# Kernel tuning notes

Hardware: AMD Instinct MI355X
Metric: run time of the kernel (lower is better)

Reference implementation:

```python
import jax, jax.numpy as jnp
import numpy as np

NUM_HEADS = 16
TOP_K = 32
NEG_INF = -1e9
EPS = 1e-8


def setup_inputs() -> dict:
    key = jax.random.key(0)
    ks = jax.random.split(key, 12)
    B, S, D = 2, 1024, 1024
    M, dk = 8192, D // NUM_HEADS
    w = lambda k: jax.random.normal(k, (D, D), jnp.float32) * 0.02
    return {
        "x": jax.random.normal(ks[0], (B, S, D), jnp.float32),
        "Wq": w(ks[1]), "bq": jnp.zeros((D,), jnp.float32),
        "Wk": w(ks[2]), "bk": jnp.zeros((D,), jnp.float32),
        "Wv": w(ks[3]), "bv": jnp.zeros((D,), jnp.float32),
        "Wo": w(ks[4]), "bo": jnp.zeros((D,), jnp.float32),
        "mem_keys": jax.random.normal(ks[5], (M, dk), jnp.float32),
        "mem_vals": jax.random.normal(ks[6], (M, dk), jnp.float32),
        "gate": jnp.zeros((1,), jnp.float32),
    }


def _normalize(v):
    return v / (jnp.linalg.norm(v, axis=-1, keepdims=True) + EPS)


def reference(x, Wq, bq, Wk, bk, Wv, bv, Wo, bo, mem_keys, mem_vals, gate):
    B, S, D = x.shape
    H = NUM_HEADS
    dk = D // H
    # projections (torch Linear: x @ W.T + b), split heads -> [B,H,S,dk]
    split = lambda t: t.reshape(B, S, H, dk).transpose(0, 2, 1, 3)
    q = split(x @ Wq.T + bq)
    k = split(x @ Wk.T + bk)
    v = split(x @ Wv.T + bv)
    # causal attention
    scores = jnp.einsum("bhqd,bhkd->bhqk", q, k) / jnp.sqrt(jnp.float32(dk))
    causal = jnp.triu(jnp.ones((S, S), bool), k=1)  # True above diagonal
    scores = jnp.where(causal, NEG_INF, scores)
    attn = jax.nn.softmax(scores, axis=-1)
    attn_out = jnp.einsum("bhqk,bhkd->bhqd", attn, v)
    attn_out = attn_out.transpose(0, 2, 1, 3).reshape(B, S, D)
    attn_out = attn_out @ Wo.T + bo
    # KNN memory retrieval on flattened per-head queries [B*H*S, dk]
    flat_q = q.reshape(-1, dk)
    sims = _normalize(flat_q) @ _normalize(mem_keys).T  # [Q, M]
    top_scores, idx = jax.lax.top_k(sims, TOP_K)        # [Q, K]
    gathered = mem_vals[idx]                            # [Q, K, dk]
    memory_out = jnp.sum(gathered * top_scores[..., None], axis=-2)  # [Q, dk]
    memory_out = memory_out.reshape(B, H, S, dk).transpose(0, 2, 1, 3).reshape(B, S, D)
    memory_out = memory_out @ Wo.T + bo
    g = jax.nn.sigmoid(gate)
    return g * memory_out + (1.0 - g) * attn_out
```

## Files before the change

kernel.cpp:

```cpp
#include <hip/hip_runtime.h>
#include <stdint.h>
#include <math.h>

#define BATCH   2
#define SEQ     1024
#define DMODEL  1024
#define NHEADS  16
#define DK      64
#define MKEYS   8192
#define NQ      (BATCH*NHEADS*SEQ)
#define THRC    2.25f
#define KPART   4
#define PKEYS2  (MKEYS/KPART)
#define PCAP    64
#define QCAP2   (KPART*PCAP)

typedef __attribute__((ext_vector_type(8))) short short8;
typedef __attribute__((ext_vector_type(4))) float f32x4;
typedef __attribute__((ext_vector_type(2))) double f64x2;
typedef __attribute__((ext_vector_type(4))) double f64x4;

__device__ __forceinline__ short f2bf(float f) {
  uint32_t u = __builtin_bit_cast(uint32_t, f);
  u = (u + 0x7fffu + ((u >> 16) & 1u)) >> 16;
  return (short)u;
}
__device__ __forceinline__ short8 ld_bf8_f32(const float* p) {
  float4 a = *(const float4*)p; float4 b = *(const float4*)(p + 4);
  short8 r;
  r[0]=f2bf(a.x); r[1]=f2bf(a.y); r[2]=f2bf(a.z); r[3]=f2bf(a.w);
  r[4]=f2bf(b.x); r[5]=f2bf(b.y); r[6]=f2bf(b.z); r[7]=f2bf(b.w);
  return r;
}

__device__ __forceinline__ unsigned long long packP(double v, int id) {
  unsigned long long b = __builtin_bit_cast(unsigned long long, v);
  b = (b & 0x8000000000000000ull) ? ~b : (b | 0x8000000000000000ull);
  return (b & ~0x1FFFull) | (unsigned long long)(8191 - id);
}
__device__ __forceinline__ double unpackV(unsigned long long P) {
  unsigned long long K = P & ~0x1FFFull;
  unsigned long long bits = (K & 0x8000000000000000ull) ? (K ^ 0x8000000000000000ull) : ~K;
  return __builtin_bit_cast(double, bits);
}

__global__ __launch_bounds__(256) void norm_keys(const float* __restrict__ mk,
                                                 double* __restrict__ knorm64,
                                                 uint16_t* __restrict__ knbf) {
  int wave = threadIdx.x >> 6, lane = threadIdx.x & 63;
  int m = blockIdx.x * 4 + wave;
  double v = (double)mk[(size_t)m * DK + lane];
  double ss = v * v;
  #pragma unroll
  for (int off = 1; off < 64; off <<= 1) ss += __shfl_xor(ss, off);
  double nv = v / (sqrt(ss) + 1e-8);
  knorm64[(size_t)m * DK + lane] = nv;
  knbf[(size_t)m * DK + lane] = (uint16_t)f2bf((float)nv);
}

__device__ __forceinline__ bool probe_decode(const f64x4 d, int base, int mul,
                                             int out[4]) {
  bool ok = true;
  #pragma unroll
  for (int r = 0; r < 4; r++) {
    int v = (int)d[r];
    int t = v - base;
    bool o = ((double)v == d[r]) && (t >= 0) && (t % mul == 0) && ((t / mul) < 16);
    out[r] = t / mul;
    ok = ok && o;
  }
  return ok;
}

__global__ __launch_bounds__(256, 4) void q64_gemm(const float* __restrict__ x,
                                                   const float* __restrict__ Wq,
                                                   const float* __restrict__ bq,
                                                   double* __restrict__ q64q,
                                                   float* __restrict__ qf32,
                                                   uint16_t* __restrict__ qb) {
  __shared__ __align__(16) float Xs[64 * 68];
  __shared__ __align__(16) float Ws[64 * 68];
  int tid = threadIdx.x, lane = tid & 63, w = tid >> 6;
  int bm = blockIdx.y * 64;
  int h = blockIdx.x;

  f64x4 z = {0.0, 0.0, 0.0, 0.0};
  f64x4 d1 = __builtin_amdgcn_mfma_f64_16x16x4f64((double)lane, 1.0, z, 0, 0, 0);
  f64x4 d2 = __builtin_amdgcn_mfma_f64_16x16x4f64(1.0, (double)lane, z, 0, 0, 0);
  int rdec[4], cdec[4];
  bool ok = probe_decode(d1, 96, 4, rdec);
  bool h1A = (bool)__all(ok ? 1 : 0);
  if (!h1A) ok = probe_decode(d1, 6, 16, rdec);
  bool aOK = h1A || (bool)__all(ok ? 1 : 0);
  ok = probe_decode(d2, 96, 4, cdec);
  bool h1B = (bool)__all(ok ? 1 : 0);
  if (!h1B) ok = probe_decode(d2, 6, 16, cdec);
  bool bOK = h1B || (bool)__all(ok ? 1 : 0);
  int iA = h1A ? (lane & 15) : (lane >> 2);
  int kA = h1A ? (lane >> 4) : (lane & 3);
  int jB = h1B ? (lane & 15) : (lane >> 2);
  int kB = h1B ? (lane >> 4) : (lane & 3);
  bool mfma_ok = aOK && bOK;
  if (mfma_ok) {
    f64x4 d3 = __builtin_amdgcn_mfma_f64_16x16x4f64(
        (double)(4 * iA + kA), (double)(jB + 16 * kB), z, 0, 0, 0);
    bool ok3 = true;
    #pragma unroll
    for (int r = 0; r < 4; r++)
      ok3 = ok3 && (d3[r] == (double)(16 * rdec[r] * cdec[r] + 384 * rdec[r] +
                                      6 * cdec[r] + 224));
    mfma_ok = (bool)__all(ok3 ? 1 : 0);
  }

  if (mfma_ok) {
    int wm = (w >> 1) * 32, wn = (w & 1) * 32;
    f64x4 acc[2][2] = {};
    for (int kt = 0; kt < 16; kt++) {
      __syncthreads();
      #pragma unroll
      for (int i = 0; i < 4; i++) {
        int c4 = tid + 256 * i;
        int r = c4 >> 4, q4 = c4 & 15;
        *(float4*)(Xs + r * 68 + q4 * 4) =
            *(const float4*)(x + (size_t)(bm + r) * DMODEL + kt * 64 + q4 * 4);
        *(float4*)(Ws + r * 68 + q4 * 4) =
            *(const float4*)(Wq + (size_t)(h * 64 + r) * DMODEL + kt * 64 + q4 * 4);
      }
      __syncthreads();
      #pragma unroll
      for (int k = 0; k < 64; k += 4) {
        double a0 = (double)Xs[(wm + iA) * 68 + k + kA];
        double a1 = (double)Xs[(wm + 16 + iA) * 68 + k + kA];
        double b0 = (double)Ws[(wn + jB) * 68 + k + kB];
        double b1 = (double)Ws[(wn + 16 + jB) * 68 + k + kB];
        acc[0][0] = __builtin_amdgcn_mfma_f64_16x16x4f64(a0, b0, acc[0][0], 0, 0, 0);
        acc[0][1] = __builtin_amdgcn_mfma_f64_16x16x4f64(a0, b1, acc[0][1], 0, 0, 0);
        acc[1][0] = __builtin_amdgcn_mfma_f64_16x16x4f64(a1, b0, acc[1][0], 0, 0, 0);
        acc[1][1] = __builtin_amdgcn_mfma_f64_16x16x4f64(a1, b1, acc[1][1], 0, 0, 0);
      }
    }
    #pragma unroll
    for (int mi = 0; mi < 2; mi++)
      #pragma unroll
      for (int ni = 0; ni < 2; ni++)
        #pragma unroll
        for (int rg = 0; rg < 4; rg++) {
          int m = bm + wm + mi * 16 + rdec[rg];
          int d = wn + ni * 16 + cdec[rg];
          int b = m >> 10, s = m & 1023;
          size_t qidx = (((size_t)(b * NHEADS + h) * SEQ) + s) * DK + d;
          double val = acc[mi][ni][rg] + (double)bq[h * DK + d];
          q64q[qidx] = val;
          float fv = (float)val;
          qf32[qidx] = fv;
          qb[qidx] = (uint16_t)f2bf(fv);
        }
  } else {
    int tx = tid & 15, ty = tid >> 4;
    double facc[4][4] = {};
    for (int kt = 0; kt < 16; kt++) {
      __syncthreads();
      #pragma unroll
      for (int i = 0; i < 4; i++) {
        int c4 = tid + 256 * i;
        int r = c4 >> 4, q4 = c4 & 15;
        *(float4*)(Xs + r * 68 + q4 * 4) =
            *(const float4*)(x + (size_t)(bm + r) * DMODEL + kt * 64 + q4 * 4);
        *(float4*)(Ws + r * 68 + q4 * 4) =
            *(const float4*)(Wq + (size_t)(h * 64 + r) * DMODEL + kt * 64 + q4 * 4);
      }
      __syncthreads();
      for (int k = 0; k < 64; k++) {
        double bv[4];
        #pragma unroll
        for (int j = 0; j < 4; j++) bv[j] = (double)Ws[(tx + 16 * j) * 68 + k];
        #pragma unroll
        for (int i = 0; i < 4; i++) {
          double a = (double)Xs[(ty * 4 + i) * 68 + k];
          #pragma unroll
          for (int j = 0; j < 4; j++) facc[i][j] = fma(a, bv[j], facc[i][j]);
        }
      }
    }
    #pragma unroll
    for (int i = 0; i < 4; i++)
      #pragma unroll
      for (int j = 0; j < 4; j++) {
        int m = bm + ty * 4 + i, d = tx + 16 * j;
        int b = m >> 10, s = m & 1023;
        size_t qidx = (((size_t)(b * NHEADS + h) * SEQ) + s) * DK + d;
        double val = facc[i][j] + (double)bq[h * DK + d];
        q64q[qidx] = val;
        float fv = (float)val;
        qf32[qidx] = fv;
        qb[qidx] = (uint16_t)f2bf(fv);
      }
  }
}

template<bool AF, bool WF>
__device__ __forceinline__ void gemm_core(const void* __restrict__ Ap,
                                          const void* __restrict__ Wp,
                                          f32x4 acc[4][4], short* As, short* Bs,
                                          int bm, int bn) {
  int tid = threadIdx.x, lane = tid & 63, w = tid >> 6;
  int wm = (w >> 1) * 64, wn = (w & 1) * 64;
  for (int kt = 0; kt < 16; kt++) {
    __syncthreads();
    #pragma unroll
    for (int i = 0; i < 4; i++) {
      int cq = tid + 256 * i;
      int r = cq >> 3, ch = cq & 7;
      size_t aoff = (size_t)(bm + r) * DMODEL + kt * 64 + ch * 8;
      size_t boff = (size_t)(bn + r) * DMODEL + kt * 64 + ch * 8;
      *(short8*)(As + r * 72 + ch * 8) = AF ? ld_bf8_f32((const float*)Ap + aoff)
                                            : *(const short8*)((const uint16_t*)Ap + aoff);
      *(short8*)(Bs + r * 72 + ch * 8) = WF ? ld_bf8_f32((const float*)Wp + boff)
                                            : *(const short8*)((const uint16_t*)Wp + boff);
    }
    __syncthreads();
    #pragma unroll
    for (int kk = 0; kk < 2; kk++) {
      short8 af[4], bfr[4];
      #pragma unroll
      for (int t = 0; t < 4; t++) {
        af[t]  = *(const short8*)(As + (wm + t * 16 + (lane & 15)) * 72 + kk * 32 + (lane >> 4) * 8);
        bfr[t] = *(const short8*)(Bs + (wn + t * 16 + (lane & 15)) * 72 + kk * 32 + (lane >> 4) * 8);
      }
      #pragma unroll
      for (int mi = 0; mi < 4; mi++)
        #pragma unroll
        for (int ni = 0; ni < 4; ni++)
          acc[mi][ni] = __builtin_amdgcn_mfma_f32_16x16x32_bf16(af[mi], bfr[ni], acc[mi][ni], 0, 0, 0);
    }
  }
}

__global__ __launch_bounds__(256) void gemm_kv(
    const float* __restrict__ x,
    const float* __restrict__ Wk, const float* __restrict__ bk,
    const float* __restrict__ Wv, const float* __restrict__ bv,
    uint16_t* __restrict__ kb, uint16_t* __restrict__ vb) {
  __shared__ __align__(16) short As[128 * 72];
  __shared__ __align__(16) short Bs[128 * 72];
  int z = blockIdx.z;
  const float* W    = z == 0 ? Wk : Wv;
  const float* bias = z == 0 ? bk : bv;
  uint16_t* outB    = z == 0 ? kb : vb;
  int bm = blockIdx.y * 128, bn = blockIdx.x * 128;
  f32x4 acc[4][4] = {};
  gemm_core<true, true>(x, W, acc, As, Bs, bm, bn);
  int lane = threadIdx.x & 63, w = threadIdx.x >> 6;
  int wm = (w >> 1) * 64, wn = (w & 1) * 64;
  #pragma unroll
  for (int mi = 0; mi < 4; mi++)
    #pragma unroll
    for (int ni = 0; ni < 4; ni++) {
      int n = bn + wn + ni * 16 + (lane & 15);
      float bvv = bias[n];
      #pragma unroll
      for (int rg = 0; rg < 4; rg++) {
        int m = bm + wm + mi * 16 + (lane >> 4) * 4 + rg;
        float v = acc[mi][ni][rg] + bvv;
        int b = m >> 10, s = m & 1023, h = n >> 6, d = n & 63;
        size_t idx = (((size_t)(b * NHEADS + h) * SEQ) + s) * DK + d;
        outB[idx] = (uint16_t)f2bf(v);
      }
    }
}

__global__ __launch_bounds__(256) void attn_fwd(
    const uint16_t* __restrict__ qb, const uint16_t* __restrict__ kb,
    const uint16_t* __restrict__ vb, float* __restrict__ attnO) {
  __shared__ __align__(16) short Ks[64 * 72];
  __shared__ __align__(16) short Vt[64 * 72];
  __shared__ __align__(16) short Ps[4][16 * 72];
  int tid = threadIdx.x, lane = tid & 63, w = tid >> 6;
  int bx = blockIdx.x;
  int qt = bx & 15, h = (bx >> 4) & 15, b = bx >> 8;
  const uint16_t* Qg = qb + (size_t)(b * NHEADS + h) * SEQ * DK;
  const uint16_t* Kg = kb + (size_t)(b * NHEADS + h) * SEQ * DK;
  const uint16_t* Vg = vb + (size_t)(b * NHEADS + h) * SEQ * DK;
  int qrow0 = qt * 64 + w * 16;
  short8 qfr[2];
  #pragma unroll
  for (int kk = 0; kk < 2; kk++)
    qfr[kk] = *(const short8*)(const void*)(Qg + (size_t)(qrow0 + (lane & 15)) * DK + kk * 32 + (lane >> 4) * 8);
  float m_i[4] = {-1e30f, -1e30f, -1e30f, -1e30f};
  float l_i[4] = {0.f, 0.f, 0.f, 0.f};
  f32x4 Oacc[4] = {};
  for (int kt = 0; kt <= qt; kt++) {
    __syncthreads();
    #pragma unroll
    for (int i = 0; i < 2; i++) {
      int cq = tid + 256 * i;
      int r = cq >> 3, ch = cq & 7;
      short8 g = *(const short8*)(const void*)(Kg + (size_t)(kt * 64 + r) * DK + ch * 8);
      *(short8*)(Ks + r * 72 + ch * 8) = g;
      short8 gv = *(const short8*)(const void*)(Vg + (size_t)(kt * 64 + r) * DK + ch * 8);
      #pragma unroll
      for (int j = 0; j < 8; j++) Vt[(ch * 8 + j) * 72 + r] = gv[j];
    }
    __syncthreads();
    f32x4 sv[4] = {};
    #pragma unroll
    for (int kk = 0; kk < 2; kk++)
      #pragma unroll
      for (int ni = 0; ni < 4; ni++) {
        short8 kf = *(const short8*)(Ks + (ni * 16 + (lane & 15)) * 72 + kk * 32 + (lane >> 4) * 8);
        sv[ni] = __builtin_amdgcn_mfma_f32_16x16x32_bf16(qfr[kk], kf, sv[ni], 0, 0, 0);
      }
    bool diag = (kt == qt);
    #pragma unroll
    for (int ni = 0; ni < 4; ni++)
      #pragma unroll
      for (int rg = 0; rg < 4; rg++) {
        float sc = sv[ni][rg] * 0.125f;
        if (diag) {
          int kcol = kt * 64 + ni * 16 + (lane & 15);
          int qrow = qrow0 + (lane >> 4) * 4 + rg;
          if (kcol > qrow) sc = -1e9f;
        }
        sv[ni][rg] = sc;
      }
    float alpha[4];
    #pragma unroll
    for (int rg = 0; rg < 4; rg++) {
      float v = fmaxf(fmaxf(sv[0][rg], sv[1][rg]), fmaxf(sv[2][rg], sv[3][rg]));
      v = fmaxf(v, __shfl_xor(v, 1)); v = fmaxf(v, __shfl_xor(v, 2));
      v = fmaxf(v, __shfl_xor(v, 4)); v = fmaxf(v, __shfl_xor(v, 8));
      float mn = fmaxf(m_i[rg], v);
      alpha[rg] = expf(m_i[rg] - mn);
      m_i[rg] = mn;
    }
    #pragma unroll
    for (int ni = 0; ni < 4; ni++)
      #pragma unroll
      for (int rg = 0; rg < 4; rg++) sv[ni][rg] = expf(sv[ni][rg] - m_i[rg]);
    #pragma unroll
    for (int rg = 0; rg < 4; rg++) {
      float s = sv[0][rg] + sv[1][rg] + sv[2][rg] + sv[3][rg];
      s += __shfl_xor(s, 1); s += __shfl_xor(s, 2);
      s += __shfl_xor(s, 4); s += __shfl_xor(s, 8);
      l_i[rg] = l_i[rg] * alpha[rg] + s;
    }
    #pragma unroll
    for (int ni = 0; ni < 4; ni++)
      #pragma unroll
      for (int rg = 0; rg < 4; rg++) Oacc[ni][rg] *= alpha[rg];
    short* Pw = &Ps[w][0];
    #pragma unroll
    for (int ni = 0; ni < 4; ni++)
      #pragma unroll
      for (int rg = 0; rg < 4; rg++)
        Pw[((lane >> 4) * 4 + rg) * 72 + ni * 16 + (lane & 15)] = f2bf(sv[ni][rg]);
    #pragma unroll
    for (int kk = 0; kk < 2; kk++) {
      short8 pa = *(const short8*)(Pw + (lane & 15) * 72 + kk * 32 + (lane >> 4) * 8);
      #pragma unroll
      for (int ni = 0; ni < 4; ni++) {
        short8 vf = *(const short8*)(Vt + (ni * 16 + (lane & 15)) * 72 + kk * 32 + (lane >> 4) * 8);
        Oacc[ni] = __builtin_amdgcn_mfma_f32_16x16x32_bf16(pa, vf, Oacc[ni], 0, 0, 0);
      }
    }
  }
  #pragma unroll
  for (int ni = 0; ni < 4; ni++)
    #pragma unroll
    for (int rg = 0; rg < 4; rg++) {
      int row = qrow0 + (lane >> 4) * 4 + rg;
      attnO[((size_t)b * SEQ + row) * DMODEL + h * DK + ni * 16 + (lane & 15)] =
          Oacc[ni][rg] / l_i[rg];
    }
}

__global__ __launch_bounds__(256) void norm_q(const float* __restrict__ qf32,
                                              float* __restrict__ t0arr) {
  int wave = threadIdx.x >> 6, lane = threadIdx.x & 63;
  int q = blockIdx.x * 4 + wave;
  float v = qf32[((size_t)q << 6) + lane];
  float ss = v * v;
  #pragma unroll
  for (int off = 1; off < 64; off <<= 1) ss += __shfl_xor(ss, off);
  if (lane == 0) t0arr[q] = (THRC / 8.0f) * sqrtf(ss);
}

__global__ __launch_bounds__(256) void knn_filter_mfma(
    const uint16_t* __restrict__ qb, const uint16_t* __restrict__ knbf,
    const float* __restrict__ t0arr,
    unsigned short* __restrict__ cand, int* __restrict__ counts) {
  __shared__ __align__(16) short Ks[64 * 68];
  int tid = threadIdx.x, lane = tid & 63, w = tid >> 6;
  int quad = lane >> 4, col = lane & 15;
  int q0 = blockIdx.y * 64;
  int p = blockIdx.x, k0 = p * PKEYS2;
  int qcol = q0 + w * 16 + col;
  short8 aq[2];
  #pragma unroll
  for (int kk = 0; kk < 2; kk++)
    aq[kk] = *(const short8*)(const void*)(qb + (size_t)qcol * DK + kk * 32 + quad * 8);
  float t0 = t0arr[qcol];
  int cntr = 0;
  for (int kt = 0; kt < PKEYS2 / 64; kt++) {
    __syncthreads();
    {
      int r = tid >> 2, ch = (tid & 3) * 2;
      const uint16_t* src = knbf + (size_t)(k0 + kt * 64 + r) * DK + ch * 8;
      *(short8*)(Ks + r * 68 + ch * 8) = *(const short8*)(const void*)src;
      *(short8*)(Ks + r * 68 + ch * 8 + 8) = *(const short8*)(const void*)(src + 8);
    }
    __syncthreads();
    f32x4 acc[4] = {};
    #pragma unroll
    for (int kk = 0; kk < 2; kk++)
      #pragma unroll
      for (int ni = 0; ni < 4; ni++) {
        short8 kf = *(const short8*)(Ks + (ni * 16 + col) * 68 + kk * 32 + quad * 8);
        acc[ni] = __builtin_amdgcn_mfma_f32_16x16x32_bf16(kf, aq[kk], acc[ni], 0, 0, 0);
      }
    unsigned pb = 0u;
    #pragma unroll
    for (int ni = 0; ni < 4; ni++)
      #pragma unroll
      for (int rg = 0; rg < 4; rg++)
        pb |= (acc[ni][rg] >= t0) ? (1u << (ni * 4 + rg)) : 0u;
    int c = __popc(pb);
    int n1 = __shfl_xor(c, 16), n2 = __shfl_xor(c, 32), n3 = __shfl_xor(c, 48);
    int o1 = quad ^ 1, o2 = quad ^ 2, o3 = quad ^ 3;
    int pre = (o1 < quad ? n1 : 0) + (o2 < quad ? n2 : 0) + (o3 < quad ? n3 : 0);
    int tot = c + n1 + n2 + n3;
    int pos = cntr + pre;
    while (pb) {
      int bi = __builtin_ctz(pb);
      pb &= pb - 1u;
      if (pos < PCAP)
        cand[((size_t)qcol * KPART + p) * PCAP + pos] =
            (unsigned short)(k0 + kt * 64 + (bi >> 2) * 16 + quad * 4 + (bi & 3));
      pos++;
    }
    cntr += tot;
  }
  if (quad == 0) {
    int cq = cntr < PCAP ? cntr : PCAP;
    counts[qcol * KPART + p] = cq;
  }
}

template<int NS>
__device__ __forceinline__ void rank_loop(const unsigned long long* cPw, int n,
                                          const unsigned long long* Pm, int* rank) {
  for (int j = 0; j < n; j++) {
    unsigned long long Pj = cPw[j];
    #pragma unroll
    for (int s = 0; s < NS; s++) rank[s] += (Pj > Pm[s]) ? 1 : 0;
  }
}

__global__ __launch_bounds__(256) void knn_select(const double* __restrict__ q64q,
                                                  const double* __restrict__ knorm64,
                                                  const unsigned short* __restrict__ cand,
                                                  const int* __restrict__ counts,
                                                  unsigned long long* __restrict__ wlE) {
  __shared__ unsigned short cid[4][QCAP2];
  __shared__ unsigned long long cP[4][QCAP2];
  __shared__ unsigned long long wl[4][32];
  int wave = threadIdx.x >> 6, lane = threadIdx.x & 63;
  int grp = lane & 7, slot = lane >> 3;
  int q = blockIdx.x * 4 + wave;
  int n = 0;
  #pragma unroll
  for (int p = 0; p < KPART; p++) {
    int c = counts[q * KPART + p]; if (c > PCAP) c = PCAP;
    if (lane < c)
      cid[wave][n + lane] = cand[((size_t)q * KPART + p) * PCAP + lane];
    n += c;
  }
  double q8[8];
  const f64x2* qrow2 = (const f64x2*)(q64q + ((size_t)q << 6));
  #pragma unroll
  for (int jj = 0; jj < 4; jj++) {
    f64x2 t = qrow2[8 * jj + grp];
    q8[2 * jj] = t[0]; q8[2 * jj + 1] = t[1];
  }
  double ssq = 0.0;
  #pragma unroll
  for (int j = 0; j < 8; j++) ssq = fma(q8[j], q8[j], ssq);
  ssq += __shfl_xor(ssq, 1); ssq += __shfl_xor(ssq, 2); ssq += __shfl_xor(ssq, 4);
  double scale = 1.0 / (sqrt(ssq) + 1e-8);
  for (int c0 = 0; c0 < n; c0 += 16) {
    int cA = c0 + slot, cB = c0 + 8 + slot;
    int idA = (cA < n) ? (int)cid[wave][cA] : 0;
    int idB = (cB < n) ? (int)cid[wave][cB] : 0;
    const f64x2* krA2 = (const f64x2*)(knorm64 + (((size_t)idA) << 6));
    const f64x2* krB2 = (const f64x2*)(knorm64 + (((size_t)idB) << 6));
    double pA = 0.0, pB = 0.0;
    #pragma unroll
    for (int jj = 0; jj < 4; jj++) {
      f64x2 a = krA2[8 * jj + grp];
      f64x2 b = krB2[8 * jj + grp];
      pA = fma(q8[2 * jj], a[0], pA); pA = fma(q8[2 * jj + 1], a[1], pA);
      pB = fma(q8[2 * jj], b[0], pB); pB = fma(q8[2 * jj + 1], b[1], pB);
    }
    pA += __shfl_xor(pA, 1); pB += __shfl_xor(pB, 1);
    pA += __shfl_xor(pA, 2); pB += __shfl_xor(pB, 2);
    pA += __shfl_xor(pA, 4); pB += __shfl_xor(pB, 4);
    if (grp == 0) {
      if (cA < n) cP[wave][cA] = packP(pA, idA);
      if (cB < n) cP[wave][cB] = packP(pB, idB);
    }
  }
  unsigned long long Pm[4]; int rank[4] = {0, 0, 0, 0};
  #pragma unroll
  for (int s = 0; s < 4; s++) {
    int idx = s * 64 + lane;
    Pm[s] = (idx < n) ? cP[wave][idx] : 0xFFFFFFFFFFFFFFFFull;
  }
  if (n > 128)      rank_loop<4>(cP[wave], n, Pm, rank);
  else if (n > 64)  rank_loop<2>(cP[wave], n, Pm, rank);
  else              rank_loop<1>(cP[wave], n, Pm, rank);
  #pragma unroll
  for (int s = 0; s < 4; s++) {
    int idx = s * 64 + lane;
    if (idx < n && rank[s] < 32) {
      int id = 8191 - (int)(Pm[s] & 0x1FFFull);
      float wgt = (float)(unpackV(Pm[s]) * scale);
      wl[wave][rank[s]] =
          ((unsigned long long)__builtin_bit_cast(unsigned, wgt) << 32) | (unsigned)id;
    }
  }
  int nsel = n < 32 ? n : 32;
  if (lane < nsel) wlE[(size_t)q * 32 + lane] = wl[wave][lane];
}

__global__ __launch_bounds__(256) void knn_gather(const unsigned long long* __restrict__ wlE,
                                                  const int* __restrict__ counts,
                                                  const float* __restrict__ mv,
                                                  const float* __restrict__ attnO,
                                                  const float* __restrict__ gate,
                                                  uint16_t* __restrict__ outb) {
  __shared__ unsigned long long wg[4][32];
  int wave = threadIdx.x >> 6, lane = threadIdx.x & 63;
  int q = blockIdx.x * 4 + wave;
  int n = 0;
  #pragma unroll
  for (int p = 0; p < KPART; p++) {
    int c = counts[q * KPART + p]; if (c > PCAP) c = PCAP;
    n += c;
  }
  int nsel = n < 32 ? n : 32;
  if (lane < 32) wg[wave][lane] = (lane < nsel) ? wlE[(size_t)q * 32 + lane] : 0;
  float accf = 0.f;
  for (int r = 0; r < nsel; r++) {
    unsigned long long e = wg[wave][r];
    int id = (int)(e & 0xFFFFFFFFull);
    float wgt = __builtin_bit_cast(float, (unsigned)(e >> 32));
    accf += wgt * mv[((size_t)id << 6) + lane];
  }
  float g = 1.f / (1.f + expf(-gate[0]));
  int b = q >> 14, h = (q >> 10) & 15, s = q & 1023;
  size_t oi = ((size_t)b * SEQ + s) * DMODEL + h * DK + lane;
  outb[oi] = (uint16_t)f2bf(g * accf + (1.f - g) * attnO[oi]);
}

__global__ __launch_bounds__(256) void gemm_out(
    const uint16_t* __restrict__ A, const float* __restrict__ W,
    const float* __restrict__ bias, float* __restrict__ out) {
  __shared__ __align__(16) short As[128 * 72];
  __shared__ __align__(16) short Bs[128 * 72];
  int bm = blockIdx.y * 128, bn = blockIdx.x * 128;
  f32x4 acc[4][4] = {};
  gemm_core<false, true>(A, W, acc, As, Bs, bm, bn);
  int lane = threadIdx.x & 63, w = threadIdx.x >> 6;
  int wm = (w >> 1) * 64, wn = (w & 1) * 64;
  #pragma unroll
  for (int mi = 0; mi < 4; mi++)
    #pragma unroll
    for (int ni = 0; ni < 4; ni++) {
      int n = bn + wn + ni * 16 + (lane & 15);
      float bvv = bias[n];
      #pragma unroll
      for (int rg = 0; rg < 4; rg++) {
        int m = bm + wm + mi * 16 + (lane >> 4) * 4 + rg;
        out[(size_t)m * DMODEL + n] = acc[mi][ni][rg] + bvv;
      }
    }
}

extern "C" void kernel_launch(void* const* d_in, const int* in_sizes, int n_in,
                              void* d_out, int out_size, void* d_ws, size_t ws_size,
                              hipStream_t stream) {
  const float* x    = (const float*)d_in[0];
  const float* Wq   = (const float*)d_in[1];
  const float* bq   = (const float*)d_in[2];
  const float* Wk   = (const float*)d_in[3];
  const float* bk   = (const float*)d_in[4];
  const float* Wv   = (const float*)d_in[5];
  const float* bv   = (const float*)d_in[6];
  const float* Wo   = (const float*)d_in[7];
  const float* bo   = (const float*)d_in[8];
  const float* mk   = (const float*)d_in[9];
  const float* mv   = (const float*)d_in[10];
  const float* gate = (const float*)d_in[11];

  char* ws = (char*)d_ws;
  double*   knorm64 = (double*)(ws);
  uint16_t* knbf    = (uint16_t*)(ws + ((size_t)4  << 20));
  float*    qf32    = (float*)(ws + ((size_t)6  << 20));
  double*   q64q    = (double*)(ws + ((size_t)14 << 20));
  uint16_t* qb      = (uint16_t*)(ws + ((size_t)30 << 20));
  uint16_t* kb      = (uint16_t*)(ws + ((size_t)34 << 20));
  uint16_t* vb      = (uint16_t*)(ws + ((size_t)38 << 20));
  float*    attnO   = (float*)(ws + ((size_t)42 << 20));
  unsigned long long* wlE = (unsigned long long*)(ws + ((size_t)50 << 20));
  uint16_t* blendb  = (uint16_t*)(ws + ((size_t)58 << 20));
  float*    t0arr   = (float*)(ws + ((size_t)62 << 20));
  int*      counts  = (int*)(ws + ((size_t)63 << 20));
  unsigned short* cnd = (unsigned short*)(ws + ((size_t)64 << 20));

  norm_keys<<<dim3(2048), dim3(256), 0, stream>>>(mk, knorm64, knbf);
  q64_gemm<<<dim3(16, 32), dim3(256), 0, stream>>>(x, Wq, bq, q64q, qf32, qb);
  gemm_kv<<<dim3(8, 16, 2), dim3(256), 0, stream>>>(x, Wk, bk, Wv, bv, kb, vb);
  attn_fwd<<<dim3(512), dim3(256), 0, stream>>>(qb, kb, vb, attnO);
  norm_q<<<dim3(8192), dim3(256), 0, stream>>>(qf32, t0arr);
  knn_filter_mfma<<<dim3(KPART, 512), dim3(256), 0, stream>>>(qb, knbf, t0arr, cnd, counts);
  knn_select<<<dim3(8192), dim3(256), 0, stream>>>(q64q, knorm64, cnd, counts, wlE);
  knn_gather<<<dim3(8192), dim3(256), 0, stream>>>(wlE, counts, mv, attnO, gate, blendb);
  gemm_out<<<dim3(8, 16), dim3(256), 0, stream>>>(blendb, Wo, bo, (float*)d_out);
}
```

Before: 452.0 us.

## Rescore KNN candidates from raw fp32 keys with per-key inverse norms

norm_keys stops writing a full fp64 normalized key matrix and stores only one fp64 inverse norm per key. knn_select now reads the raw fp32 memory keys, converts them to double, takes the dot product and multiplies by the stored inverse norm. It also processes four candidates per slot per iteration instead of two and changes the per-lane query layout to contiguous chunks. This halves gathered key bytes and removes the 4 MB knorm64 write, at the cost of a different rounding order that could change tie-breaking in top-k selection.

```diff
diff --git a/kernel.cpp b/kernel.cpp
--- a/kernel.cpp
+++ b/kernel.cpp
@@ -45,7 +45,7 @@
 }
 
 __global__ __launch_bounds__(256) void norm_keys(const float* __restrict__ mk,
-                                                 double* __restrict__ knorm64,
+                                                 double* __restrict__ invn64,
                                                  uint16_t* __restrict__ knbf) {
   int wave = threadIdx.x >> 6, lane = threadIdx.x & 63;
   int m = blockIdx.x * 4 + wave;
@@ -53,9 +53,9 @@
   double ss = v * v;
   #pragma unroll
   for (int off = 1; off < 64; off <<= 1) ss += __shfl_xor(ss, off);
-  double nv = v / (sqrt(ss) + 1e-8);
-  knorm64[(size_t)m * DK + lane] = nv;
-  knbf[(size_t)m * DK + lane] = (uint16_t)f2bf((float)nv);
+  double inv = 1.0 / (sqrt(ss) + 1e-8);
+  knbf[(size_t)m * DK + lane] = (uint16_t)f2bf((float)(v * inv));
+  if (lane == 0) invn64[m] = inv;
 }
 
 __device__ __forceinline__ bool probe_decode(const f64x4 d, int base, int mul,
@@ -457,7 +457,8 @@
 }
 
 __global__ __launch_bounds__(256) void knn_select(const double* __restrict__ q64q,
-                                                  const double* __restrict__ knorm64,
+                                                  const float* __restrict__ mk,
+                                                  const double* __restrict__ invn,
                                                   const unsigned short* __restrict__ cand,
                                                   const int* __restrict__ counts,
                                                   unsigned long long* __restrict__ wlE) {
@@ -476,37 +477,46 @@
     n += c;
   }
   double q8[8];
-  const f64x2* qrow2 = (const f64x2*)(q64q + ((size_t)q << 6));
-  #pragma unroll
-  for (int jj = 0; jj < 4; jj++) {
-    f64x2 t = qrow2[8 * jj + grp];
-    q8[2 * jj] = t[0]; q8[2 * jj + 1] = t[1];
+  {
+    const f64x2* qrow2 = (const f64x2*)(q64q + ((size_t)q << 6) + 8 * grp);
+    #pragma unroll
+    for (int j = 0; j < 4; j++) { f64x2 t = qrow2[j]; q8[2*j] = t[0]; q8[2*j+1] = t[1]; }
   }
   double ssq = 0.0;
   #pragma unroll
   for (int j = 0; j < 8; j++) ssq = fma(q8[j], q8[j], ssq);
   ssq += __shfl_xor(ssq, 1); ssq += __shfl_xor(ssq, 2); ssq += __shfl_xor(ssq, 4);
   double scale = 1.0 / (sqrt(ssq) + 1e-8);
-  for (int c0 = 0; c0 < n; c0 += 16) {
-    int cA = c0 + slot, cB = c0 + 8 + slot;
-    int idA = (cA < n) ? (int)cid[wave][cA] : 0;
-    int idB = (cB < n) ? (int)cid[wave][cB] : 0;
-    const f64x2* krA2 = (const f64x2*)(knorm64 + (((size_t)idA) << 6));
-    const f64x2* krB2 = (const f64x2*)(knorm64 + (((size_t)idB) << 6));
-    double pA = 0.0, pB = 0.0;
-    #pragma unroll
-    for (int jj = 0; jj < 4; jj++) {
-      f64x2 a = krA2[8 * jj + grp];
-      f64x2 b = krB2[8 * jj + grp];
-      pA = fma(q8[2 * jj], a[0], pA); pA = fma(q8[2 * jj + 1], a[1], pA);
-      pB = fma(q8[2 * jj], b[0], pB); pB = fma(q8[2 * jj + 1], b[1], pB);
-    }
-    pA += __shfl_xor(pA, 1); pB += __shfl_xor(pB, 1);
-    pA += __shfl_xor(pA, 2); pB += __shfl_xor(pB, 2);
-    pA += __shfl_xor(pA, 4); pB += __shfl_xor(pB, 4);
+  for (int c0 = 0; c0 < n; c0 += 32) {
+    int cc[4], id[4];
+    #pragma unroll
+    for (int u = 0; u < 4; u++) {
+      cc[u] = c0 + 8 * u + slot;
+      id[u] = (cc[u] < n) ? (int)cid[wave][cc[u]] : 0;
+    }
+    double pv[4];
+    #pragma unroll
+    for (int u = 0; u < 4; u++) {
+      const float* kr = mk + (((size_t)id[u]) << 6) + 8 * grp;
+      float4 a = *(const float4*)kr;
+      float4 b = *(const float4*)(kr + 4);
+      double s = 0.0;
+      s = fma(q8[0], (double)a.x, s); s = fma(q8[1], (double)a.y, s);
+      s = fma(q8[2], (double)a.z, s); s = fma(q8[3], (double)a.w, s);
+      s = fma(q8[4], (double)b.x, s); s = fma(q8[5], (double)b.y, s);
+      s = fma(q8[6], (double)b.z, s); s = fma(q8[7], (double)b.w, s);
+      pv[u] = s;
+    }
+    #pragma unroll
+    for (int u = 0; u < 4; u++) {
+      pv[u] += __shfl_xor(pv[u], 1);
+      pv[u] += __shfl_xor(pv[u], 2);
+      pv[u] += __shfl_xor(pv[u], 4);
+    }
     if (grp == 0) {
-      if (cA < n) cP[wave][cA] = packP(pA, idA);
-      if (cB < n) cP[wave][cB] = packP(pB, idB);
+      #pragma unroll
+      for (int u = 0; u < 4; u++)
+        if (cc[u] < n) cP[wave][cc[u]] = packP(pv[u] * invn[id[u]], id[u]);
     }
   }
   unsigned long long Pm[4]; int rank[4] = {0, 0, 0, 0};
@@ -603,7 +613,7 @@
   const float* gate = (const float*)d_in[11];
 
   char* ws = (char*)d_ws;
-  double*   knorm64 = (double*)(ws);
+  double*   invn64  = (double*)(ws);
   uint16_t* knbf    = (uint16_t*)(ws + ((size_t)4  << 20));
   float*    qf32    = (float*)(ws + ((size_t)6  << 20));
   double*   q64q    = (double*)(ws + ((size_t)14 << 20));
@@ -617,13 +627,13 @@
   int*      counts  = (int*)(ws + ((size_t)63 << 20));
   unsigned short* cnd = (unsigned short*)(ws + ((size_t)64 << 20));
 
-  norm_keys<<<dim3(2048), dim3(256), 0, stream>>>(mk, knorm64, knbf);
+  norm_keys<<<dim3(2048), dim3(256), 0, stream>>>(mk, invn64, knbf);
   q64_gemm<<<dim3(16, 32), dim3(256), 0, stream>>>(x, Wq, bq, q64q, qf32, qb);
   gemm_kv<<<dim3(8, 16, 2), dim3(256), 0, stream>>>(x, Wk, bk, Wv, bv, kb, vb);
   attn_fwd<<<dim3(512), dim3(256), 0, stream>>>(qb, kb, vb, attnO);
   norm_q<<<dim3(8192), dim3(256), 0, stream>>>(qf32, t0arr);
   knn_filter_mfma<<<dim3(KPART, 512), dim3(256), 0, stream>>>(qb, knbf, t0arr, cnd, counts);
-  knn_select<<<dim3(8192), dim3(256), 0, stream>>>(q64q, knorm64, cnd, counts, wlE);
+  knn_select<<<dim3(8192), dim3(256), 0, stream>>>(q64q, mk, invn64, cnd, counts, wlE);
   knn_gather<<<dim3(8192), dim3(256), 0, stream>>>(wlE, counts, mv, attnO, gate, blendb);
   gemm_out<<<dim3(8, 16), dim3(256), 0, stream>>>(blendb, Wo, bo, (float*)d_out);
 }
```

Result: slower. 463.0 us (+2.4%).
